# Kernel optimization log

Measured on AMD Instinct MI355X. Metric: run time of the kernel, lower is better.

The kernel has to match this reference:

```python
import jax, jax.numpy as jnp
import numpy as np

N = 50000      # nodes
E = 250000     # edges
NG = 2500      # graphs
H = 32         # atom_dim
ND = 32        # node feature dim
ED = 16        # edge feature dim
CONV_N = 3     # message passing steps
EMB_STEPS = 3  # Set2Set processing steps


def setup_inputs() -> dict:
    key = jax.random.key(0)
    ks = jax.random.split(key, 16)
    w = lambda k, shape, s=0.05: jax.random.normal(k, shape, jnp.float32) * s
    return {
        "x": jax.random.normal(ks[0], (N, ND), jnp.float32),
        "edge_index": jax.random.randint(ks[1], (2, E), 0, N),
        "edge_attr": jax.random.normal(ks[2], (E, ED), jnp.float32),
        "batch": jnp.sort(jax.random.randint(ks[3], (N,), 0, NG)),
        "lin_w": w(ks[4], (ND, H)), "lin_b": jnp.zeros((H,), jnp.float32),
        "e_w1": w(ks[5], (ED, 2 * H)), "e_b1": jnp.zeros((2 * H,), jnp.float32),
        "e_w2": w(ks[6], (2 * H, H * H)), "e_b2": jnp.zeros((H * H,), jnp.float32),
        "gru_w_ih": w(ks[7], (3 * H, H)), "gru_w_hh": w(ks[8], (3 * H, H)),
        "gru_b_ih": jnp.zeros((3 * H,), jnp.float32), "gru_b_hh": jnp.zeros((3 * H,), jnp.float32),
        "lstm_w_ih": w(ks[9], (4 * H, 2 * H)), "lstm_w_hh": w(ks[10], (4 * H, H)),
        "lstm_b_ih": jnp.zeros((4 * H,), jnp.float32), "lstm_b_hh": jnp.zeros((4 * H,), jnp.float32),
        "pred_w": w(ks[11], (2 * H, 1)), "pred_b": jnp.zeros((1,), jnp.float32),
    }


def _mpnn_forward(x, edge_attr, lin_w, lin_b, e_w1, e_b1, e_w2, e_b2,
                  gru_w_ih, gru_w_hh, gru_b_ih, gru_b_hh,
                  lstm_w_ih, lstm_w_hh, lstm_b_ih, lstm_b_hh,
                  pred_w, pred_b, edge_index, batch):
    src, dst = edge_index[0], edge_index[1]
    # initial node embedding: relu(Linear(node_dim -> atom_dim))
    out = jax.nn.relu(x @ lin_w + lin_b)            # [N, H]
    h = out                                         # GRU hidden state [N, H]

    # edge-conditioned weights (edge MLP output is constant across conv steps)
    e_h = jax.nn.relu(edge_attr @ e_w1 + e_b1)      # [E, 2H]
    W_e = (e_h @ e_w2 + e_b2).reshape(E, H, H)      # [E, H, H]

    # mean-aggregation denominator per target node
    deg = jax.ops.segment_sum(jnp.ones((E,), out.dtype), dst, num_segments=N)
    denom = jnp.maximum(deg, 1.0)[:, None]          # [N, 1]

    for _ in range(CONV_N):
        # NNConv message: m_e = x_src @ W_e, mean-scattered to dst
        msg = jnp.einsum('eh,eho->eo', out[src], W_e)                   # [E, H]
        agg = jax.ops.segment_sum(msg, dst, num_segments=N) / denom     # [N, H]
        m = jax.nn.relu(agg)
        # single GRU cell step (seq_len=1)
        gi = m @ gru_w_ih.T + gru_b_ih              # [N, 3H]
        gh = h @ gru_w_hh.T + gru_b_hh              # [N, 3H]
        i_r, i_z, i_n = jnp.split(gi, 3, axis=-1)
        h_r, h_z, h_n = jnp.split(gh, 3, axis=-1)
        r = jax.nn.sigmoid(i_r + h_r)
        z = jax.nn.sigmoid(i_z + h_z)
        n = jnp.tanh(i_n + r * h_n)
        h = (1.0 - z) * n + z * h
        out = h

    # Set2Set pooling over graphs (only last embedding used, residual='last')
    q_star = jnp.zeros((NG, 2 * H), out.dtype)
    hl = jnp.zeros((NG, H), out.dtype)
    cl = jnp.zeros((NG, H), out.dtype)
    for _ in range(EMB_STEPS):
        g = q_star @ lstm_w_ih.T + lstm_b_ih + hl @ lstm_w_hh.T + lstm_b_hh  # [NG, 4H]
        gi_, gf_, gg_, go_ = jnp.split(g, 4, axis=-1)
        i_g = jax.nn.sigmoid(gi_)
        f_g = jax.nn.sigmoid(gf_)
        g_g = jnp.tanh(gg_)
        o_g = jax.nn.sigmoid(go_)
        cl = f_g * cl + i_g * g_g
        hl = o_g * jnp.tanh(cl)
        q = hl                                       # [NG, H]
        e = jnp.sum(out * q[batch], axis=-1)         # [N]
        e_max = jax.ops.segment_max(e, batch, num_segments=NG)
        e_exp = jnp.exp(e - e_max[batch])
        e_den = jax.ops.segment_sum(e_exp, batch, num_segments=NG)
        a = e_exp / e_den[batch]                     # softmax within each graph
        r_pool = jax.ops.segment_sum(a[:, None] * out, batch, num_segments=NG)  # [NG, H]
        q_star = jnp.concatenate([q, r_pool], axis=-1)

    pred = q_star @ pred_w + pred_b                  # [NG, 1]
    return pred.reshape(-1)


def reference(x, edge_index, edge_attr, batch, lin_w, lin_b, e_w1, e_b1, e_w2, e_b2,
              gru_w_ih, gru_w_hh, gru_b_ih, gru_b_hh,
              lstm_w_ih, lstm_w_hh, lstm_b_ih, lstm_b_hh, pred_w, pred_b):
    return _mpnn_forward(x, edge_attr, lin_w, lin_b, e_w1, e_b1, e_w2, e_b2,
                         gru_w_ih, gru_w_hh, gru_b_ih, gru_b_hh,
                         lstm_w_ih, lstm_w_hh, lstm_b_ih, lstm_b_hh,
                         pred_w, pred_b, edge_index, batch)
```

## Files before the change

### kernel.cpp

```cpp
#include <hip/hip_runtime.h>
#include <hip/hip_bf16.h>

namespace {
constexpr int kN = 50000;
constexpr int kE = 250000;
constexpr int kG = 2500;

__device__ __forceinline__ float sigmoidf_(float x) { return 1.0f / (1.0f + expf(-x)); }

__global__ void k_starts(const int* __restrict__ batch, int* __restrict__ starts) {
  int g = blockIdx.x * blockDim.x + threadIdx.x;
  if (g > kG) return;
  int lo = 0, hi = kN;
  while (lo < hi) {
    int mid = (lo + hi) >> 1;
    if (batch[mid] < g) lo = mid + 1; else hi = mid;
  }
  starts[g] = lo;
}

__global__ __launch_bounds__(256) void k_node_init(const float* __restrict__ x,
                                                   const float* __restrict__ lin_w,
                                                   const float* __restrict__ lin_b,
                                                   float* __restrict__ h) {
  __shared__ float ws[32 * 32];
  __shared__ float bs[32];
  for (int i = threadIdx.x; i < 1024; i += 256) ws[i] = lin_w[i];
  if (threadIdx.x < 32) bs[threadIdx.x] = lin_b[threadIdx.x];
  __syncthreads();
  int n = blockIdx.x * 256 + threadIdx.x;
  if (n >= kN) return;
  float xv[32];
  const float4* xp = (const float4*)(x + (size_t)n * 32);
#pragma unroll
  for (int i = 0; i < 8; ++i) {
    float4 v = xp[i];
    xv[4 * i + 0] = v.x; xv[4 * i + 1] = v.y; xv[4 * i + 2] = v.z; xv[4 * i + 3] = v.w;
  }
  float acc[32];
#pragma unroll
  for (int o = 0; o < 32; ++o) acc[o] = bs[o];
  for (int i = 0; i < 32; ++i) {
    float a = xv[i];
    const float4* wr = (const float4*)&ws[i * 32];
#pragma unroll
    for (int o4 = 0; o4 < 8; ++o4) {
      float4 w = wr[o4];
      acc[4 * o4 + 0] = fmaf(a, w.x, acc[4 * o4 + 0]);
      acc[4 * o4 + 1] = fmaf(a, w.y, acc[4 * o4 + 1]);
      acc[4 * o4 + 2] = fmaf(a, w.z, acc[4 * o4 + 2]);
      acc[4 * o4 + 3] = fmaf(a, w.w, acc[4 * o4 + 3]);
    }
  }
  float4* hp = (float4*)(h + (size_t)n * 32);
#pragma unroll
  for (int i = 0; i < 8; ++i) {
    float4 v;
    v.x = fmaxf(acc[4 * i + 0], 0.f);
    v.y = fmaxf(acc[4 * i + 1], 0.f);
    v.z = fmaxf(acc[4 * i + 2], 0.f);
    v.w = fmaxf(acc[4 * i + 3], 0.f);
    hp[i] = v;
  }
}

__global__ __launch_bounds__(256) void k_edge_h(const float* __restrict__ ea,
                                                const float* __restrict__ w1,
                                                const float* __restrict__ b1,
                                                float* __restrict__ eh) {
  __shared__ float ws[16 * 64];
  __shared__ float bs[64];
  for (int i = threadIdx.x; i < 1024; i += 256) ws[i] = w1[i];
  if (threadIdx.x < 64) bs[threadIdx.x] = b1[threadIdx.x];
  __syncthreads();
  int e = blockIdx.x * 256 + threadIdx.x;
  if (e >= kE) return;
  float av[16];
  const float4* ap = (const float4*)(ea + (size_t)e * 16);
#pragma unroll
  for (int i = 0; i < 4; ++i) {
    float4 v = ap[i];
    av[4 * i + 0] = v.x; av[4 * i + 1] = v.y; av[4 * i + 2] = v.z; av[4 * i + 3] = v.w;
  }
  float acc[64];
#pragma unroll
  for (int o = 0; o < 64; ++o) acc[o] = bs[o];
  for (int i = 0; i < 16; ++i) {
    float a = av[i];
    const float4* wr = (const float4*)&ws[i * 64];
#pragma unroll
    for (int o4 = 0; o4 < 16; ++o4) {
      float4 w = wr[o4];
      acc[4 * o4 + 0] = fmaf(a, w.x, acc[4 * o4 + 0]);
      acc[4 * o4 + 1] = fmaf(a, w.y, acc[4 * o4 + 1]);
      acc[4 * o4 + 2] = fmaf(a, w.z, acc[4 * o4 + 2]);
      acc[4 * o4 + 3] = fmaf(a, w.w, acc[4 * o4 + 3]);
    }
  }
  float4* op = (float4*)(eh + (size_t)e * 64);
#pragma unroll
  for (int i = 0; i < 16; ++i) {
    float4 v;
    v.x = fmaxf(acc[4 * i + 0], 0.f);
    v.y = fmaxf(acc[4 * i + 1], 0.f);
    v.z = fmaxf(acc[4 * i + 2], 0.f);
    v.w = fmaxf(acc[4 * i + 3], 0.f);
    op[i] = v;
  }
}

__global__ void k_deg(const int* __restrict__ dst, float* __restrict__ denom) {
  int e = blockIdx.x * blockDim.x + threadIdx.x;
  if (e < kE) atomicAdd(&denom[dst[e]], 1.0f);
}

__global__ void k_hist(const int* __restrict__ src, int* __restrict__ cnt) {
  int e = blockIdx.x * blockDim.x + threadIdx.x;
  if (e < kE) atomicAdd(&cnt[src[e]], 1);
}

__global__ __launch_bounds__(1024) void k_scan(const int* __restrict__ cnt, int* __restrict__ offs) {
  __shared__ int wsum[16];
  __shared__ int wpre[16];
  __shared__ int carry_s;
  const int tid = threadIdx.x;
  const int lane = tid & 63, wv = tid >> 6;
  if (tid == 0) carry_s = 0;
  __syncthreads();
  for (int base = 0; base < kN; base += 1024) {
    int i = base + tid;
    int v = (i < kN) ? cnt[i] : 0;
    int x = v;
#pragma unroll
    for (int d = 1; d < 64; d <<= 1) {
      int t = __shfl_up(x, d, 64);
      if (lane >= d) x += t;
    }
    if (lane == 63) wsum[wv] = x;
    __syncthreads();
    if (wv == 0) {
      int y = (lane < 16) ? wsum[lane] : 0;
#pragma unroll
      for (int d = 1; d < 16; d <<= 1) {
        int t = __shfl_up(y, d, 64);
        if (lane >= d && lane < 16) y += t;
      }
      if (lane < 16) wpre[lane] = y - wsum[lane];
    }
    __syncthreads();
    int carry = carry_s;
    if (i < kN) offs[i] = carry + wpre[wv] + (x - v);
    __syncthreads();
    if (tid == 0) carry_s = carry + wpre[15] + wsum[15];
    __syncthreads();
  }
  if (tid == 0) offs[kN] = carry_s;
}

__global__ void k_scatter(const int* __restrict__ src, const int* __restrict__ dst,
                          const int* __restrict__ offs, int* __restrict__ cur,
                          int* __restrict__ es_e, int* __restrict__ es_src,
                          int* __restrict__ es_dst) {
  int e = blockIdx.x * blockDim.x + threadIdx.x;
  if (e >= kE) return;
  int s = src[e];
  int pos = offs[s] + atomicAdd(&cur[s], 1);
  es_e[pos] = e;
  es_src[pos] = s;
  es_dst[pos] = dst[e];
}

__global__ __launch_bounds__(256, 2) void k_conv(const float* __restrict__ h,
                                                 const float* __restrict__ eh,
                                                 const float* __restrict__ w2,
                                                 const float* __restrict__ b2,
                                                 const int* __restrict__ es_e,
                                                 const int* __restrict__ es_src,
                                                 const int* __restrict__ es_dst,
                                                 const int* __restrict__ offs,
                                                 float* __restrict__ agg) {
  __shared__ float Ts[8][64][32];
  __shared__ float hs[8][32];
  __shared__ float hb2[8][32];
  const int n0 = blockIdx.x * 8;
  const int t = threadIdx.x;
  const int kg = t >> 5;
  const int o = t & 31;
  hs[kg][o] = h[(size_t)(n0 + kg) * 32 + o];
  __syncthreads();
  {
    float acc = 0.f;
#pragma unroll
    for (int a = 0; a < 32; ++a) acc = fmaf(hs[kg][a], b2[a * 32 + o], acc);
    hb2[kg][o] = acc;
  }
  float acc[8][8];
#pragma unroll
  for (int n = 0; n < 8; ++n)
#pragma unroll
    for (int kk = 0; kk < 8; ++kk) acc[n][kk] = 0.f;
  const float* w2p = w2 + (size_t)kg * 8 * 1024 + o;
#pragma unroll 2
  for (int a4 = 0; a4 < 8; ++a4) {
    float4 hv[8];
#pragma unroll
    for (int n = 0; n < 8; ++n) hv[n] = *(const float4*)&hs[n][a4 * 4];
#pragma unroll
    for (int j = 0; j < 4; ++j) {
      const int a = a4 * 4 + j;
      float w[8];
#pragma unroll
      for (int kk = 0; kk < 8; ++kk) w[kk] = w2p[(size_t)kk * 1024 + a * 32];
#pragma unroll
      for (int n = 0; n < 8; ++n) {
        float hval = (j == 0) ? hv[n].x : (j == 1) ? hv[n].y : (j == 2) ? hv[n].z : hv[n].w;
#pragma unroll
        for (int kk = 0; kk < 8; ++kk) acc[n][kk] = fmaf(hval, w[kk], acc[n][kk]);
      }
    }
  }
#pragma unroll
  for (int n = 0; n < 8; ++n)
#pragma unroll
    for (int kk = 0; kk < 8; ++kk) Ts[n][kg * 8 + kk][o] = acc[n][kk];
  __syncthreads();
  const int es = offs[n0], ee = offs[n0 + 8];
  for (int ei = es + kg; ei < ee; ei += 8) {
    const int e = es_e[ei];
    const int nl = es_src[ei] - n0;
    const int d = es_dst[ei];
    const float ehA = eh[(size_t)e * 64 + o];
    const float ehB = eh[(size_t)e * 64 + 32 + o];
    float m = hb2[nl][o];
#pragma unroll
    for (int k = 0; k < 32; ++k) m = fmaf(__shfl(ehA, k, 32), Ts[nl][k][o], m);
#pragma unroll
    for (int k = 0; k < 32; ++k) m = fmaf(__shfl(ehB, k, 32), Ts[nl][32 + k][o], m);
    atomicAdd(&agg[(size_t)d * 32 + o], m);
  }
}

__global__ __launch_bounds__(256) void k_gru(float* __restrict__ h, const float* __restrict__ agg,
                                             const float* __restrict__ denom,
                                             const float* __restrict__ Wih, const float* __restrict__ Whh,
                                             const float* __restrict__ bih, const float* __restrict__ bhh) {
  __shared__ float wih_s[96 * 32];
  __shared__ float whh_s[96 * 32];
  __shared__ float bih_s[96], bhh_s[96];
  for (int i = threadIdx.x; i < 96 * 32; i += 256) { wih_s[i] = Wih[i]; whh_s[i] = Whh[i]; }
  for (int i = threadIdx.x; i < 96; i += 256) { bih_s[i] = bih[i]; bhh_s[i] = bhh[i]; }
  __syncthreads();
  int n = blockIdx.x * 256 + threadIdx.x;
  if (n >= kN) return;
  float dn = fmaxf(denom[n], 1.0f);
  float m[32], hv[32];
  const float4* ap = (const float4*)(agg + (size_t)n * 32);
  const float4* hp = (const float4*)(h + (size_t)n * 32);
#pragma unroll
  for (int i = 0; i < 8; ++i) {
    float4 a = ap[i];
    m[4 * i + 0] = fmaxf(a.x / dn, 0.f);
    m[4 * i + 1] = fmaxf(a.y / dn, 0.f);
    m[4 * i + 2] = fmaxf(a.z / dn, 0.f);
    m[4 * i + 3] = fmaxf(a.w / dn, 0.f);
    float4 b = hp[i];
    hv[4 * i + 0] = b.x; hv[4 * i + 1] = b.y; hv[4 * i + 2] = b.z; hv[4 * i + 3] = b.w;
  }
  float rr[32], zz[32];
#pragma unroll 4
  for (int j = 0; j < 32; ++j) {
    float accA = bih_s[j], accB = bhh_s[j];
    const float4* wi = (const float4*)&wih_s[j * 32];
    const float4* wh = (const float4*)&whh_s[j * 32];
#pragma unroll
    for (int i = 0; i < 8; ++i) {
      float4 a = wi[i], b = wh[i];
      accA = fmaf(m[4 * i + 0], a.x, accA); accA = fmaf(m[4 * i + 1], a.y, accA);
      accA = fmaf(m[4 * i + 2], a.z, accA); accA = fmaf(m[4 * i + 3], a.w, accA);
      accB = fmaf(hv[4 * i + 0], b.x, accB); accB = fmaf(hv[4 * i + 1], b.y, accB);
      accB = fmaf(hv[4 * i + 2], b.z, accB); accB = fmaf(hv[4 * i + 3], b.w, accB);
    }
    rr[j] = sigmoidf_(accA + accB);
  }
#pragma unroll 4
  for (int j = 0; j < 32; ++j) {
    int row = 32 + j;
    float accA = bih_s[row], accB = bhh_s[row];
    const float4* wi = (const float4*)&wih_s[row * 32];
    const float4* wh = (const float4*)&whh_s[row * 32];
#pragma unroll
    for (int i = 0; i < 8; ++i) {
      float4 a = wi[i], b = wh[i];
      accA = fmaf(m[4 * i + 0], a.x, accA); accA = fmaf(m[4 * i + 1], a.y, accA);
      accA = fmaf(m[4 * i + 2], a.z, accA); accA = fmaf(m[4 * i + 3], a.w, accA);
      accB = fmaf(hv[4 * i + 0], b.x, accB); accB = fmaf(hv[4 * i + 1], b.y, accB);
      accB = fmaf(hv[4 * i + 2], b.z, accB); accB = fmaf(hv[4 * i + 3], b.w, accB);
    }
    zz[j] = sigmoidf_(accA + accB);
  }
#pragma unroll 4
  for (int j = 0; j < 32; ++j) {
    int row = 64 + j;
    float accA = bih_s[row], accB = bhh_s[row];
    const float4* wi = (const float4*)&wih_s[row * 32];
    const float4* wh = (const float4*)&whh_s[row * 32];
#pragma unroll
    for (int i = 0; i < 8; ++i) {
      float4 a = wi[i], b = wh[i];
      accA = fmaf(m[4 * i + 0], a.x, accA); accA = fmaf(m[4 * i + 1], a.y, accA);
      accA = fmaf(m[4 * i + 2], a.z, accA); accA = fmaf(m[4 * i + 3], a.w, accA);
      accB = fmaf(hv[4 * i + 0], b.x, accB); accB = fmaf(hv[4 * i + 1], b.y, accB);
      accB = fmaf(hv[4 * i + 2], b.z, accB); accB = fmaf(hv[4 * i + 3], b.w, accB);
    }
    float ng = tanhf(accA + rr[j] * accB);
    zz[j] = (1.f - zz[j]) * ng + zz[j] * hv[j];
  }
  float4* hw = (float4*)(h + (size_t)n * 32);
#pragma unroll
  for (int i = 0; i < 8; ++i)
    hw[i] = make_float4(zz[4 * i + 0], zz[4 * i + 1], zz[4 * i + 2], zz[4 * i + 3]);
}

__global__ __launch_bounds__(256) void k_lstm(const float* __restrict__ hl_in, const float* __restrict__ cl_in,
                                              const float* __restrict__ rpool,
                                              float* __restrict__ hl_out, float* __restrict__ cl_out,
                                              const float* __restrict__ Wih, const float* __restrict__ Whh,
                                              const float* __restrict__ bih, const float* __restrict__ bhh) {
  __shared__ float wih_s[128 * 64];
  __shared__ float whh_s[128 * 32];
  __shared__ float bsum[128];
  for (int i = threadIdx.x; i < 128 * 64; i += 256) wih_s[i] = Wih[i];
  for (int i = threadIdx.x; i < 128 * 32; i += 256) whh_s[i] = Whh[i];
  for (int i = threadIdx.x; i < 128; i += 256) bsum[i] = bih[i] + bhh[i];
  __syncthreads();
  int t = blockIdx.x * 256 + threadIdx.x;
  int g = t >> 5, j = t & 31;
  if (g >= kG) return;
  float qa[32], qb[32];
  const float4* hp = (const float4*)(hl_in + (size_t)g * 32);
  const float4* rp = (const float4*)(rpool + (size_t)g * 32);
#pragma unroll
  for (int i = 0; i < 8; ++i) {
    float4 a = hp[i];
    qa[4 * i + 0] = a.x; qa[4 * i + 1] = a.y; qa[4 * i + 2] = a.z; qa[4 * i + 3] = a.w;
    float4 b = rp[i];
    qb[4 * i + 0] = b.x; qb[4 * i + 1] = b.y; qb[4 * i + 2] = b.z; qb[4 * i + 3] = b.w;
  }
  float v[4];
#pragma unroll
  for (int gate = 0; gate < 4; ++gate) {
    int row = gate * 32 + j;
    float acc = bsum[row];
    const float4* wi = (const float4*)&wih_s[row * 64];
    const float4* wh = (const float4*)&whh_s[row * 32];
#pragma unroll
    for (int i = 0; i < 8; ++i) {
      float4 a = wi[i];
      acc = fmaf(qa[4 * i + 0], a.x, acc); acc = fmaf(qa[4 * i + 1], a.y, acc);
      acc = fmaf(qa[4 * i + 2], a.z, acc); acc = fmaf(qa[4 * i + 3], a.w, acc);
    }
#pragma unroll
    for (int i = 0; i < 8; ++i) {
      float4 a = wi[8 + i];
      acc = fmaf(qb[4 * i + 0], a.x, acc); acc = fmaf(qb[4 * i + 1], a.y, acc);
      acc = fmaf(qb[4 * i + 2], a.z, acc); acc = fmaf(qb[4 * i + 3], a.w, acc);
    }
#pragma unroll
    for (int i = 0; i < 8; ++i) {
      float4 a = wh[i];
      acc = fmaf(qa[4 * i + 0], a.x, acc); acc = fmaf(qa[4 * i + 1], a.y, acc);
      acc = fmaf(qa[4 * i + 2], a.z, acc); acc = fmaf(qa[4 * i + 3], a.w, acc);
    }
    v[gate] = acc;
  }
  float ig = sigmoidf_(v[0]);
  float fg = sigmoidf_(v[1]);
  float gg = tanhf(v[2]);
  float og = sigmoidf_(v[3]);
  float c = fg * cl_in[(size_t)g * 32 + j] + ig * gg;
  cl_out[(size_t)g * 32 + j] = c;
  hl_out[(size_t)g * 32 + j] = og * tanhf(c);
}

__global__ void k_attn(const float* __restrict__ h, const float* __restrict__ hl,
                       const int* __restrict__ starts, float* __restrict__ rpool) {
  int wv = (blockIdx.x * blockDim.x + threadIdx.x) >> 6;
  if (wv >= kG) return;
  int lane = threadIdx.x & 63;
  int o = lane & 31;
  int s = starts[wv], e = starts[wv + 1];
  float q = hl[(size_t)wv * 32 + o];
  float mx = -3.0e38f;
  for (int n0 = s; n0 < e; n0 += 2) {
    int n = n0 + (lane >> 5);
    float val = (n < e) ? h[(size_t)n * 32 + o] * q : 0.f;
#pragma unroll
    for (int d = 16; d; d >>= 1) val += __shfl_xor(val, d, 32);
    if (n < e) mx = fmaxf(mx, val);
  }
  mx = fmaxf(mx, __shfl_xor(mx, 32));
  float den = 0.f, rp = 0.f;
  for (int n0 = s; n0 < e; n0 += 2) {
    int n = n0 + (lane >> 5);
    float hvo = 0.f, val = 0.f;
    if (n < e) { hvo = h[(size_t)n * 32 + o]; val = hvo * q; }
#pragma unroll
    for (int d = 16; d; d >>= 1) val += __shfl_xor(val, d, 32);
    if (n < e) {
      float p = expf(val - mx);
      den += p;
      rp = fmaf(p, hvo, rp);
    }
  }
  den += __shfl_xor(den, 32);
  rp += __shfl_xor(rp, 32);
  if (lane < 32) rpool[(size_t)wv * 32 + o] = (e > s) ? rp / den : 0.f;
}

__global__ void k_pred(const float* __restrict__ hl_f, const float* __restrict__ rpool,
                       const float* __restrict__ pw, const float* __restrict__ pb,
                       float* __restrict__ out) {
  int g = blockIdx.x * blockDim.x + threadIdx.x;
  if (g >= kG) return;
  float acc = pb[0];
#pragma unroll 4
  for (int i = 0; i < 32; ++i) acc = fmaf(hl_f[(size_t)g * 32 + i], pw[i], acc);
#pragma unroll 4
  for (int i = 0; i < 32; ++i) acc = fmaf(rpool[(size_t)g * 32 + i], pw[32 + i], acc);
  out[g] = acc;
}

}

extern "C" void kernel_launch(void* const* d_in, const int* in_sizes, int n_in,
                              void* d_out, int out_size, void* d_ws, size_t ws_size,
                              hipStream_t stream) {
  const float* x     = (const float*)d_in[0];
  const int*   eidx  = (const int*)d_in[1];
  const float* eattr = (const float*)d_in[2];
  const int*   batch = (const int*)d_in[3];
  const float* lin_w = (const float*)d_in[4];
  const float* lin_b = (const float*)d_in[5];
  const float* e_w1  = (const float*)d_in[6];
  const float* e_b1  = (const float*)d_in[7];
  const float* e_w2  = (const float*)d_in[8];
  const float* e_b2  = (const float*)d_in[9];
  const float* gwih  = (const float*)d_in[10];
  const float* gwhh  = (const float*)d_in[11];
  const float* gbih  = (const float*)d_in[12];
  const float* gbhh  = (const float*)d_in[13];
  const float* lwih  = (const float*)d_in[14];
  const float* lwhh  = (const float*)d_in[15];
  const float* lbih  = (const float*)d_in[16];
  const float* lbhh  = (const float*)d_in[17];
  const float* pw    = (const float*)d_in[18];
  const float* pb    = (const float*)d_in[19];
  const int* srcp = eidx;
  const int* dstp = eidx + kE;

  float* ws = (float*)d_ws;
  size_t off = 0;
  auto alloc = [&](size_t nel) {
    float* p = ws + off;
    off += (nel + 255) & ~(size_t)255;
    return p;
  };
  float* hbuf  = alloc((size_t)kN * 32);
  float* agg   = alloc((size_t)kN * 32);
  float* denom = alloc(kN);
  float* ehb   = alloc((size_t)kE * 64);
  float* hl0   = alloc((size_t)kG * 32);
  float* hl1   = alloc((size_t)kG * 32);
  float* cl0   = alloc((size_t)kG * 32);
  float* cl1   = alloc((size_t)kG * 32);
  float* rpool = alloc((size_t)kG * 32);
  int* starts  = (int*)alloc(kG + 1);
  int* cnt     = (int*)alloc(kN);
  int* cur     = (int*)alloc(kN);
  int* offs    = (int*)alloc(kN + 1);
  int* es_e    = (int*)alloc(kE);
  int* es_src  = (int*)alloc(kE);
  int* es_dst  = (int*)alloc(kE);
  if (ws_size / 4 < off) return;

  hipMemsetAsync(denom, 0, (size_t)kN * 4, stream);
  hipMemsetAsync(hl0, 0, (size_t)kG * 32 * 4, stream);
  hipMemsetAsync(cl0, 0, (size_t)kG * 32 * 4, stream);
  hipMemsetAsync(rpool, 0, (size_t)kG * 32 * 4, stream);
  hipMemsetAsync(cnt, 0, (size_t)kN * 4, stream);
  hipMemsetAsync(cur, 0, (size_t)kN * 4, stream);

  k_starts<<<(kG + 1 + 255) / 256, 256, 0, stream>>>(batch, starts);
  k_node_init<<<(kN + 255) / 256, 256, 0, stream>>>(x, lin_w, lin_b, hbuf);
  k_edge_h<<<(kE + 255) / 256, 256, 0, stream>>>(eattr, e_w1, e_b1, ehb);
  k_deg<<<(kE + 255) / 256, 256, 0, stream>>>(dstp, denom);

  k_hist<<<(kE + 255) / 256, 256, 0, stream>>>(srcp, cnt);
  k_scan<<<1, 1024, 0, stream>>>(cnt, offs);
  k_scatter<<<(kE + 255) / 256, 256, 0, stream>>>(srcp, dstp, offs, cur, es_e, es_src, es_dst);

  for (int step = 0; step < 3; ++step) {
    hipMemsetAsync(agg, 0, (size_t)kN * 32 * 4, stream);
    k_conv<<<kN / 8, 256, 0, stream>>>(hbuf, ehb, e_w2, e_b2, es_e, es_src, es_dst, offs, agg);
    k_gru<<<(kN + 255) / 256, 256, 0, stream>>>(hbuf, agg, denom, gwih, gwhh, gbih, gbhh);
  }

  float* hls[2] = {hl0, hl1};
  float* cls[2] = {cl0, cl1};
  int a = 0;
  for (int t = 0; t < 3; ++t) {
    int b = a ^ 1;
    k_lstm<<<(kG * 32 + 255) / 256, 256, 0, stream>>>(hls[a], cls[a], rpool, hls[b], cls[b],
                                                      lwih, lwhh, lbih, lbhh);
    k_attn<<<(kG * 64 + 255) / 256, 256, 0, stream>>>(hbuf, hls[b], starts, rpool);
    a = b;
  }
  k_pred<<<(kG + 255) / 256, 256, 0, stream>>>(hls[a], rpool, pw, pb, (float*)d_out);
}
```

Measured before the change: 1.049 ms.

## Rework edge conv tiling with transposed W2, fuse Set2Set loop and degree histogram

The edge conv kernel now handles 16 nodes per block instead of 8. It uses a pre-transposed e_w2 so each thread can issue float4 weight loads, and it processes the 64-wide hidden dimension in two halves through a smaller padded shared tile. The Set2Set LSTM, attention and prediction kernels are merged into one kernel with one wavefront per graph that loops over all three steps in registers, which removes several launches and the intermediate state buffers. The degree and source-histogram atomic kernels are merged into one launch. The trade-off is a second pass over each node block's edges, which re-gathers the edge indices and adds extra atomics to agg, plus heavier per-thread register use in the conv kernel.

New measurement: 1.099 ms. +4.7%, slower.

```diff
diff --git a/kernel.cpp b/kernel.cpp
--- a/kernel.cpp
+++ b/kernel.cpp
@@ -5,6 +5,7 @@
 constexpr int kN = 50000;
 constexpr int kE = 250000;
 constexpr int kG = 2500;
+constexpr int NB = 16;
 
 __device__ __forceinline__ float sigmoidf_(float x) { return 1.0f / (1.0f + expf(-x)); }
 
@@ -109,14 +110,13 @@
   }
 }
 
-__global__ void k_deg(const int* __restrict__ dst, float* __restrict__ denom) {
+__global__ void k_deg_hist(const int* __restrict__ dst, const int* __restrict__ src,
+                           float* __restrict__ denom, int* __restrict__ cnt) {
   int e = blockIdx.x * blockDim.x + threadIdx.x;
-  if (e < kE) atomicAdd(&denom[dst[e]], 1.0f);
-}
-
-__global__ void k_hist(const int* __restrict__ src, int* __restrict__ cnt) {
-  int e = blockIdx.x * blockDim.x + threadIdx.x;
-  if (e < kE) atomicAdd(&cnt[src[e]], 1);
+  if (e < kE) {
+    atomicAdd(&denom[dst[e]], 1.0f);
+    atomicAdd(&cnt[src[e]], 1);
+  }
 }
 
 __global__ __launch_bounds__(1024) void k_scan(const int* __restrict__ cnt, int* __restrict__ offs) {
@@ -170,73 +170,97 @@
   es_dst[pos] = dst[e];
 }
 
-__global__ __launch_bounds__(256, 2) void k_conv(const float* __restrict__ h,
-                                                 const float* __restrict__ eh,
-                                                 const float* __restrict__ w2,
-                                                 const float* __restrict__ b2,
-                                                 const int* __restrict__ es_e,
-                                                 const int* __restrict__ es_src,
-                                                 const int* __restrict__ es_dst,
-                                                 const int* __restrict__ offs,
-                                                 float* __restrict__ agg) {
-  __shared__ float Ts[8][64][32];
-  __shared__ float hs[8][32];
-  __shared__ float hb2[8][32];
-  const int n0 = blockIdx.x * 8;
+__global__ void k_w2t(const float* __restrict__ w2, float* __restrict__ w2t) {
+  int i = blockIdx.x * 256 + threadIdx.x;
+  if (i >= 65536) return;
+  int k = i & 63, oa = i >> 6;
+  int o = oa & 31, a = oa >> 5;
+  w2t[i] = w2[(size_t)k * 1024 + a * 32 + o];
+}
+
+__global__ __launch_bounds__(256, 2) void k_conv2(const float* __restrict__ h,
+                                                  const float* __restrict__ eh,
+                                                  const float* __restrict__ w2t,
+                                                  const float* __restrict__ b2,
+                                                  const int* __restrict__ es_e,
+                                                  const int* __restrict__ es_src,
+                                                  const int* __restrict__ es_dst,
+                                                  const int* __restrict__ offs,
+                                                  float* __restrict__ agg) {
+  __shared__ float Ts[NB][32][36];
+  __shared__ float hs[NB][32];
+  __shared__ float hb2[NB][32];
+  const int n0 = blockIdx.x * NB;
   const int t = threadIdx.x;
+  {
+    int n = t >> 5, o = t & 31;
+    hs[n][o]     = h[(size_t)(n0 + n) * 32 + o];
+    hs[n + 8][o] = h[(size_t)(n0 + n + 8) * 32 + o];
+  }
+  __syncthreads();
+  {
+    int n = t >> 5, o = t & 31;
+    float a0 = 0.f, a1 = 0.f;
+    for (int a = 0; a < 32; ++a) {
+      float b = b2[a * 32 + o];
+      a0 = fmaf(hs[n][a], b, a0);
+      a1 = fmaf(hs[n + 8][a], b, a1);
+    }
+    hb2[n][o] = a0;
+    hb2[n + 8][o] = a1;
+  }
+  const int og = t >> 3;
+  const int kq = t & 7;
   const int kg = t >> 5;
-  const int o = t & 31;
-  hs[kg][o] = h[(size_t)(n0 + kg) * 32 + o];
-  __syncthreads();
-  {
-    float acc = 0.f;
-#pragma unroll
-    for (int a = 0; a < 32; ++a) acc = fmaf(hs[kg][a], b2[a * 32 + o], acc);
-    hb2[kg][o] = acc;
-  }
-  float acc[8][8];
-#pragma unroll
-  for (int n = 0; n < 8; ++n)
-#pragma unroll
-    for (int kk = 0; kk < 8; ++kk) acc[n][kk] = 0.f;
-  const float* w2p = w2 + (size_t)kg * 8 * 1024 + o;
-#pragma unroll 2
-  for (int a4 = 0; a4 < 8; ++a4) {
-    float4 hv[8];
-#pragma unroll
-    for (int n = 0; n < 8; ++n) hv[n] = *(const float4*)&hs[n][a4 * 4];
-#pragma unroll
-    for (int j = 0; j < 4; ++j) {
-      const int a = a4 * 4 + j;
-      float w[8];
-#pragma unroll
-      for (int kk = 0; kk < 8; ++kk) w[kk] = w2p[(size_t)kk * 1024 + a * 32];
-#pragma unroll
-      for (int n = 0; n < 8; ++n) {
-        float hval = (j == 0) ? hv[n].x : (j == 1) ? hv[n].y : (j == 2) ? hv[n].z : hv[n].w;
-#pragma unroll
-        for (int kk = 0; kk < 8; ++kk) acc[n][kk] = fmaf(hval, w[kk], acc[n][kk]);
+  const int ol = t & 31;
+  const int es = offs[n0], ee = offs[n0 + NB];
+  const float* wp = w2t + og * 64 + kq * 4;
+
+  for (int kh = 0; kh < 2; ++kh) {
+    float4 acc[NB];
+#pragma unroll
+    for (int n = 0; n < NB; ++n) acc[n] = make_float4(0.f, 0.f, 0.f, 0.f);
+    const float* wph = wp + kh * 32;
+    for (int a4 = 0; a4 < 8; ++a4) {
+      const float* wa = wph + (size_t)(a4 * 4) * 2048;
+      float4 w0 = *(const float4*)(wa);
+      float4 w1 = *(const float4*)(wa + 2048);
+      float4 w2v = *(const float4*)(wa + 4096);
+      float4 w3 = *(const float4*)(wa + 6144);
+#pragma unroll
+      for (int n = 0; n < NB; ++n) {
+        float4 hv = *(const float4*)&hs[n][a4 * 4];
+        acc[n].x = fmaf(hv.x, w0.x, acc[n].x); acc[n].y = fmaf(hv.x, w0.y, acc[n].y);
+        acc[n].z = fmaf(hv.x, w0.z, acc[n].z); acc[n].w = fmaf(hv.x, w0.w, acc[n].w);
+        acc[n].x = fmaf(hv.y, w1.x, acc[n].x); acc[n].y = fmaf(hv.y, w1.y, acc[n].y);
+        acc[n].z = fmaf(hv.y, w1.z, acc[n].z); acc[n].w = fmaf(hv.y, w1.w, acc[n].w);
+        acc[n].x = fmaf(hv.z, w2v.x, acc[n].x); acc[n].y = fmaf(hv.z, w2v.y, acc[n].y);
+        acc[n].z = fmaf(hv.z, w2v.z, acc[n].z); acc[n].w = fmaf(hv.z, w2v.w, acc[n].w);
+        acc[n].x = fmaf(hv.w, w3.x, acc[n].x); acc[n].y = fmaf(hv.w, w3.y, acc[n].y);
+        acc[n].z = fmaf(hv.w, w3.z, acc[n].z); acc[n].w = fmaf(hv.w, w3.w, acc[n].w);
       }
     }
-  }
-#pragma unroll
-  for (int n = 0; n < 8; ++n)
-#pragma unroll
-    for (int kk = 0; kk < 8; ++kk) Ts[n][kg * 8 + kk][o] = acc[n][kk];
-  __syncthreads();
-  const int es = offs[n0], ee = offs[n0 + 8];
-  for (int ei = es + kg; ei < ee; ei += 8) {
-    const int e = es_e[ei];
-    const int nl = es_src[ei] - n0;
-    const int d = es_dst[ei];
-    const float ehA = eh[(size_t)e * 64 + o];
-    const float ehB = eh[(size_t)e * 64 + 32 + o];
-    float m = hb2[nl][o];
-#pragma unroll
-    for (int k = 0; k < 32; ++k) m = fmaf(__shfl(ehA, k, 32), Ts[nl][k][o], m);
-#pragma unroll
-    for (int k = 0; k < 32; ++k) m = fmaf(__shfl(ehB, k, 32), Ts[nl][32 + k][o], m);
-    atomicAdd(&agg[(size_t)d * 32 + o], m);
+    if (kh) __syncthreads();
+#pragma unroll
+    for (int n = 0; n < NB; ++n) *(float4*)&Ts[n][og][kq * 4] = acc[n];
+    __syncthreads();
+    for (int ei = es + kg; ei < ee; ei += 8) {
+      const int e = es_e[ei];
+      const int nl = es_src[ei] - n0;
+      const int d = es_dst[ei];
+      const float ehv = eh[(size_t)e * 64 + kh * 32 + ol];
+      float m = kh ? 0.f : hb2[nl][ol];
+      const float* tp = &Ts[nl][ol][0];
+#pragma unroll
+      for (int j4 = 0; j4 < 8; ++j4) {
+        float4 tv = *(const float4*)(tp + j4 * 4);
+        m = fmaf(__shfl(ehv, j4 * 4 + 0, 32), tv.x, m);
+        m = fmaf(__shfl(ehv, j4 * 4 + 1, 32), tv.y, m);
+        m = fmaf(__shfl(ehv, j4 * 4 + 2, 32), tv.z, m);
+        m = fmaf(__shfl(ehv, j4 * 4 + 3, 32), tv.w, m);
+      }
+      atomicAdd(&agg[(size_t)d * 32 + ol], m);
+    }
   }
 }
 
@@ -321,113 +345,74 @@
     hw[i] = make_float4(zz[4 * i + 0], zz[4 * i + 1], zz[4 * i + 2], zz[4 * i + 3]);
 }
 
-__global__ __launch_bounds__(256) void k_lstm(const float* __restrict__ hl_in, const float* __restrict__ cl_in,
-                                              const float* __restrict__ rpool,
-                                              float* __restrict__ hl_out, float* __restrict__ cl_out,
-                                              const float* __restrict__ Wih, const float* __restrict__ Whh,
-                                              const float* __restrict__ bih, const float* __restrict__ bhh) {
-  __shared__ float wih_s[128 * 64];
-  __shared__ float whh_s[128 * 32];
+__global__ __launch_bounds__(256) void k_s2s(const float* __restrict__ h,
+                                             const int* __restrict__ starts,
+                                             const float* __restrict__ lwih,
+                                             const float* __restrict__ lwhh,
+                                             const float* __restrict__ lbih,
+                                             const float* __restrict__ lbhh,
+                                             const float* __restrict__ pw,
+                                             const float* __restrict__ pb,
+                                             float* __restrict__ out) {
+  __shared__ float wih_s[128][65];
+  __shared__ float whh_s[128][33];
   __shared__ float bsum[128];
-  for (int i = threadIdx.x; i < 128 * 64; i += 256) wih_s[i] = Wih[i];
-  for (int i = threadIdx.x; i < 128 * 32; i += 256) whh_s[i] = Whh[i];
-  for (int i = threadIdx.x; i < 128; i += 256) bsum[i] = bih[i] + bhh[i];
-  __syncthreads();
-  int t = blockIdx.x * 256 + threadIdx.x;
-  int g = t >> 5, j = t & 31;
+  for (int i = threadIdx.x; i < 128 * 64; i += 256) wih_s[i >> 6][i & 63] = lwih[i];
+  for (int i = threadIdx.x; i < 128 * 32; i += 256) whh_s[i >> 5][i & 31] = lwhh[i];
+  for (int i = threadIdx.x; i < 128; i += 256) bsum[i] = lbih[i] + lbhh[i];
+  __syncthreads();
+  const int g = blockIdx.x * 4 + (threadIdx.x >> 6);
   if (g >= kG) return;
-  float qa[32], qb[32];
-  const float4* hp = (const float4*)(hl_in + (size_t)g * 32);
-  const float4* rp = (const float4*)(rpool + (size_t)g * 32);
-#pragma unroll
-  for (int i = 0; i < 8; ++i) {
-    float4 a = hp[i];
-    qa[4 * i + 0] = a.x; qa[4 * i + 1] = a.y; qa[4 * i + 2] = a.z; qa[4 * i + 3] = a.w;
-    float4 b = rp[i];
-    qb[4 * i + 0] = b.x; qb[4 * i + 1] = b.y; qb[4 * i + 2] = b.z; qb[4 * i + 3] = b.w;
-  }
-  float v[4];
-#pragma unroll
-  for (int gate = 0; gate < 4; ++gate) {
-    int row = gate * 32 + j;
-    float acc = bsum[row];
-    const float4* wi = (const float4*)&wih_s[row * 64];
-    const float4* wh = (const float4*)&whh_s[row * 32];
-#pragma unroll
-    for (int i = 0; i < 8; ++i) {
-      float4 a = wi[i];
-      acc = fmaf(qa[4 * i + 0], a.x, acc); acc = fmaf(qa[4 * i + 1], a.y, acc);
-      acc = fmaf(qa[4 * i + 2], a.z, acc); acc = fmaf(qa[4 * i + 3], a.w, acc);
-    }
-#pragma unroll
-    for (int i = 0; i < 8; ++i) {
-      float4 a = wi[8 + i];
-      acc = fmaf(qb[4 * i + 0], a.x, acc); acc = fmaf(qb[4 * i + 1], a.y, acc);
-      acc = fmaf(qb[4 * i + 2], a.z, acc); acc = fmaf(qb[4 * i + 3], a.w, acc);
-    }
-#pragma unroll
-    for (int i = 0; i < 8; ++i) {
-      float4 a = wh[i];
-      acc = fmaf(qa[4 * i + 0], a.x, acc); acc = fmaf(qa[4 * i + 1], a.y, acc);
-      acc = fmaf(qa[4 * i + 2], a.z, acc); acc = fmaf(qa[4 * i + 3], a.w, acc);
-    }
-    v[gate] = acc;
-  }
-  float ig = sigmoidf_(v[0]);
-  float fg = sigmoidf_(v[1]);
-  float gg = tanhf(v[2]);
-  float og = sigmoidf_(v[3]);
-  float c = fg * cl_in[(size_t)g * 32 + j] + ig * gg;
-  cl_out[(size_t)g * 32 + j] = c;
-  hl_out[(size_t)g * 32 + j] = og * tanhf(c);
-}
-
-__global__ void k_attn(const float* __restrict__ h, const float* __restrict__ hl,
-                       const int* __restrict__ starts, float* __restrict__ rpool) {
-  int wv = (blockIdx.x * blockDim.x + threadIdx.x) >> 6;
-  if (wv >= kG) return;
-  int lane = threadIdx.x & 63;
-  int o = lane & 31;
-  int s = starts[wv], e = starts[wv + 1];
-  float q = hl[(size_t)wv * 32 + o];
-  float mx = -3.0e38f;
-  for (int n0 = s; n0 < e; n0 += 2) {
-    int n = n0 + (lane >> 5);
-    float val = (n < e) ? h[(size_t)n * 32 + o] * q : 0.f;
-#pragma unroll
-    for (int d = 16; d; d >>= 1) val += __shfl_xor(val, d, 32);
-    if (n < e) mx = fmaxf(mx, val);
-  }
-  mx = fmaxf(mx, __shfl_xor(mx, 32));
-  float den = 0.f, rp = 0.f;
-  for (int n0 = s; n0 < e; n0 += 2) {
-    int n = n0 + (lane >> 5);
-    float hvo = 0.f, val = 0.f;
-    if (n < e) { hvo = h[(size_t)n * 32 + o]; val = hvo * q; }
-#pragma unroll
-    for (int d = 16; d; d >>= 1) val += __shfl_xor(val, d, 32);
-    if (n < e) {
-      float p = expf(val - mx);
-      den += p;
-      rp = fmaf(p, hvo, rp);
-    }
-  }
-  den += __shfl_xor(den, 32);
-  rp += __shfl_xor(rp, 32);
-  if (lane < 32) rpool[(size_t)wv * 32 + o] = (e > s) ? rp / den : 0.f;
-}
-
-__global__ void k_pred(const float* __restrict__ hl_f, const float* __restrict__ rpool,
-                       const float* __restrict__ pw, const float* __restrict__ pb,
-                       float* __restrict__ out) {
-  int g = blockIdx.x * blockDim.x + threadIdx.x;
-  if (g >= kG) return;
-  float acc = pb[0];
-#pragma unroll 4
-  for (int i = 0; i < 32; ++i) acc = fmaf(hl_f[(size_t)g * 32 + i], pw[i], acc);
-#pragma unroll 4
-  for (int i = 0; i < 32; ++i) acc = fmaf(rpool[(size_t)g * 32 + i], pw[32 + i], acc);
-  out[g] = acc;
+  const int lane = threadIdx.x & 63;
+  const int o = lane & 31;
+  const int r1 = lane, r2 = lane + 64;
+  const int s = starts[g], e = starts[g + 1];
+  float c = 0.f, hl = 0.f, rp = 0.f;
+  for (int step = 0; step < 3; ++step) {
+    float v1 = bsum[r1], v2 = bsum[r2];
+    for (int i = 0; i < 32; ++i) {
+      float hli = __shfl(hl, i, 64);
+      float rpi = __shfl(rp, i, 64);
+      v1 = fmaf(wih_s[r1][i], hli, v1);
+      v1 = fmaf(wih_s[r1][32 + i], rpi, v1);
+      v1 = fmaf(whh_s[r1][i], hli, v1);
+      v2 = fmaf(wih_s[r2][i], hli, v2);
+      v2 = fmaf(wih_s[r2][32 + i], rpi, v2);
+      v2 = fmaf(whh_s[r2][i], hli, v2);
+    }
+    float fg = sigmoidf_(__shfl(v1, 32 + o, 64));
+    float og_ = sigmoidf_(__shfl(v2, 32 + o, 64));
+    float ig = sigmoidf_(v1);
+    float gg = tanhf(v2);
+    c = fg * c + ig * gg;
+    hl = og_ * tanhf(c);
+    float q = __shfl(hl, o, 64);
+    float mx = -3.0e38f;
+    for (int nn = s; nn < e; nn += 2) {
+      int n = nn + (lane >> 5);
+      float val = (n < e) ? h[(size_t)n * 32 + o] * q : 0.f;
+#pragma unroll
+      for (int d = 16; d; d >>= 1) val += __shfl_xor(val, d, 32);
+      if (n < e) mx = fmaxf(mx, val);
+    }
+    mx = fmaxf(mx, __shfl_xor(mx, 32, 64));
+    float den = 0.f, racc = 0.f;
+    for (int nn = s; nn < e; nn += 2) {
+      int n = nn + (lane >> 5);
+      float hvo = 0.f, val = 0.f;
+      if (n < e) { hvo = h[(size_t)n * 32 + o]; val = hvo * q; }
+#pragma unroll
+      for (int d = 16; d; d >>= 1) val += __shfl_xor(val, d, 32);
+      if (n < e) { float p = expf(val - mx); den += p; racc = fmaf(p, hvo, racc); }
+    }
+    den += __shfl_xor(den, 32, 64);
+    racc += __shfl_xor(racc, 32, 64);
+    rp = (e > s) ? racc / den : 0.f;
+  }
+  float acc = __shfl(hl, o, 64) * pw[o] + rp * pw[32 + o];
+#pragma unroll
+  for (int d = 16; d; d >>= 1) acc += __shfl_xor(acc, d, 32);
+  if (lane == 0) out[g] = acc + pb[0];
 }
 
 }
@@ -469,11 +454,7 @@
   float* agg   = alloc((size_t)kN * 32);
   float* denom = alloc(kN);
   float* ehb   = alloc((size_t)kE * 64);
-  float* hl0   = alloc((size_t)kG * 32);
-  float* hl1   = alloc((size_t)kG * 32);
-  float* cl0   = alloc((size_t)kG * 32);
-  float* cl1   = alloc((size_t)kG * 32);
-  float* rpool = alloc((size_t)kG * 32);
+  float* w2t   = alloc(65536);
   int* starts  = (int*)alloc(kG + 1);
   int* cnt     = (int*)alloc(kN);
   int* cur     = (int*)alloc(kN);
@@ -484,36 +465,23 @@
   if (ws_size / 4 < off) return;
 
   hipMemsetAsync(denom, 0, (size_t)kN * 4, stream);
-  hipMemsetAsync(hl0, 0, (size_t)kG * 32 * 4, stream);
-  hipMemsetAsync(cl0, 0, (size_t)kG * 32 * 4, stream);
-  hipMemsetAsync(rpool, 0, (size_t)kG * 32 * 4, stream);
   hipMemsetAsync(cnt, 0, (size_t)kN * 4, stream);
   hipMemsetAsync(cur, 0, (size_t)kN * 4, stream);
 
   k_starts<<<(kG + 1 + 255) / 256, 256, 0, stream>>>(batch, starts);
   k_node_init<<<(kN + 255) / 256, 256, 0, stream>>>(x, lin_w, lin_b, hbuf);
   k_edge_h<<<(kE + 255) / 256, 256, 0, stream>>>(eattr, e_w1, e_b1, ehb);
-  k_deg<<<(kE + 255) / 256, 256, 0, stream>>>(dstp, denom);
-
-  k_hist<<<(kE + 255) / 256, 256, 0, stream>>>(srcp, cnt);
+  k_deg_hist<<<(kE + 255) / 256, 256, 0, stream>>>(dstp, srcp, denom, cnt);
   k_scan<<<1, 1024, 0, stream>>>(cnt, offs);
   k_scatter<<<(kE + 255) / 256, 256, 0, stream>>>(srcp, dstp, offs, cur, es_e, es_src, es_dst);
+  k_w2t<<<65536 / 256, 256, 0, stream>>>(e_w2, w2t);
 
   for (int step = 0; step < 3; ++step) {
     hipMemsetAsync(agg, 0, (size_t)kN * 32 * 4, stream);
-    k_conv<<<kN / 8, 256, 0, stream>>>(hbuf, ehb, e_w2, e_b2, es_e, es_src, es_dst, offs, agg);
+    k_conv2<<<kN / NB, 256, 0, stream>>>(hbuf, ehb, w2t, e_b2, es_e, es_src, es_dst, offs, agg);
     k_gru<<<(kN + 255) / 256, 256, 0, stream>>>(hbuf, agg, denom, gwih, gwhh, gbih, gbhh);
   }
 
-  float* hls[2] = {hl0, hl1};
-  float* cls[2] = {cl0, cl1};
-  int a = 0;
-  for (int t = 0; t < 3; ++t) {
-    int b = a ^ 1;
-    k_lstm<<<(kG * 32 + 255) / 256, 256, 0, stream>>>(hls[a], cls[a], rpool, hls[b], cls[b],
-                                                      lwih, lwhh, lbih, lbhh);
-    k_attn<<<(kG * 64 + 255) / 256, 256, 0, stream>>>(hbuf, hls[b], starts, rpool);
-    a = b;
-  }
-  k_pred<<<(kG + 255) / 256, 256, 0, stream>>>(hls[a], rpool, pw, pb, (float*)d_out);
-}
+  k_s2s<<<(kG + 3) / 4, 256, 0, stream>>>(hbuf, starts, lwih, lwhh, lbih, lbhh, pw, pb,
+                                          (float*)d_out);
+}
```
